# Kernel tuning notes

Hardware: AMD Instinct MI355X
Metric: run time of the kernel (lower is better)

Reference implementation:

```python
import jax, jax.numpy as jnp
import numpy as np

B, T, HID = 4, 4096, 768
H, D = 12, 64
N_HASHES = 2
BUCKET_SIZE = T // 32          # reformer repo config: max_seq_len // 32 = 128
N_BUCKETS = T // BUCKET_SIZE   # 32
SELF_ATTN_VALUE = -5e4         # reformer_pytorch TOKEN_SELF_ATTN_VALUE
MASK_VALUE = -1e9


def lsh_attention(X, mask_bool, W_qk, W_v, rotations):
    # X: [b, t, hid]; rotations: [d, n_hashes, n_buckets//2] (shared across batch & heads)
    b, t, _ = X.shape
    d, n_hashes, half_nb = rotations.shape
    n_buckets = 2 * half_nb
    h = W_qk.shape[0] // d
    scale = d ** -0.5

    qk = X @ W_qk.T            # shared query/key projection (bias-free in reformer_pytorch)
    v = X @ W_v.T

    def merge_heads(x):  # [b,t,h*d] -> [b*h, t, d]
        return x.reshape(b, t, h, d).transpose(0, 2, 1, 3).reshape(b * h, t, d)

    qk, v = merge_heads(qk), merge_heads(v)
    maskbh = jnp.repeat(mask_bool, h, axis=0)          # [bh, t]

    # --- LSH bucketing ---
    rotated = jnp.einsum('btf,fhi->bhti', qk, rotations)          # [bh, nh, t, nb/2]
    rotated = jnp.concatenate([rotated, -rotated], axis=-1)       # [bh, nh, t, nb]
    buckets = jnp.argmax(rotated, axis=-1)                        # [bh, nh, t]
    offsets = (jnp.arange(n_hashes) * n_buckets)[None, :, None]
    buckets = (buckets + offsets).reshape(b * h, n_hashes * t)

    # --- stable sort by (bucket, position) ---
    total = n_hashes * t
    ticker = jnp.arange(total)[None, :]
    buckets_and_t = buckets * t + (ticker % t)
    sticker = jnp.argsort(buckets_and_t, axis=-1)   # stable
    undo = jnp.argsort(sticker, axis=-1)
    st = sticker % t                                 # original positions, sorted order

    sqk = jnp.take_along_axis(qk, st[..., None], axis=1)
    sv = jnp.take_along_axis(v, st[..., None], axis=1)
    smask = jnp.take_along_axis(maskbh, st, axis=1)

    # --- chunk; each chunk attends to itself + previous chunk ---
    n_chunks = n_hashes * n_buckets
    cl = total // n_chunks                                  # == bucket_size
    bq_t = st.reshape(b * h, n_chunks, cl)
    bqk = sqk.reshape(b * h, n_chunks, cl, d)
    bv = sv.reshape(b * h, n_chunks, cl, d)
    bmask = smask.reshape(b * h, n_chunks, cl)

    bq = bqk
    bk = bqk / jnp.clip(jnp.linalg.norm(bqk, axis=-1, keepdims=True), 1e-12)

    def look_one_back(x):
        return jnp.concatenate([x, jnp.roll(x, 1, axis=1)], axis=2)

    bk, bv = look_one_back(bk), look_one_back(bv)
    bkv_t = look_one_back(bq_t)
    bkv_mask = look_one_back(bmask)

    dots = jnp.einsum('bnie,bnje->bnij', bq, bk) * scale    # [bh, n_chunks, cl, 2cl]
    pad = bmask[..., :, None] & bkv_mask[..., None, :]
    dots = jnp.where(pad, dots, MASK_VALUE)
    self_mask = bq_t[..., :, None] == bkv_t[..., None, :]
    dots = jnp.where(self_mask, SELF_ATTN_VALUE, dots)

    lse = jax.scipy.special.logsumexp(dots, axis=-1, keepdims=True)
    probs = jnp.exp(dots - lse)
    bo = jnp.einsum('bnij,bnje->bnie', probs, bv)

    # --- unsort and combine hash rounds via softmax over round logsumexps ---
    so = bo.reshape(b * h, total, d)
    slogits = lse.reshape(b * h, total)
    o = jnp.take_along_axis(so, undo[..., None], axis=1)
    logits = jnp.take_along_axis(slogits, undo, axis=1)

    o = o.reshape(b * h, n_hashes, t, d)
    logits = logits.reshape(b * h, n_hashes, t, 1)
    round_probs = jnp.exp(logits - jax.scipy.special.logsumexp(logits, axis=1, keepdims=True))
    out = jnp.sum(o * round_probs, axis=1)                  # [bh, t, d]
    return out.reshape(b, h, t, d).transpose(0, 2, 1, 3).reshape(b, t, h * d)


def setup_inputs() -> dict:
    key = jax.random.key(0)
    ks = jax.random.split(key, 8)
    s = 1.0 / np.sqrt(HID)
    return {
        'X': jax.random.normal(ks[0], (B, T, HID), jnp.float32),
        'mask': jnp.ones((B, T), jnp.float32),
        'W_qk': jax.random.uniform(ks[1], (H * D, HID), jnp.float32, -s, s),
        'W_v': jax.random.uniform(ks[2], (H * D, HID), jnp.float32, -s, s),
        'rotations': jax.random.normal(ks[3], (D, N_HASHES, N_BUCKETS // 2), jnp.float32),
        'W_to': jax.random.uniform(ks[4], (HID, H * D), jnp.float32, -s, s),
        'b_to': jnp.zeros((HID,), jnp.float32),
        'W_o': jax.random.uniform(ks[5], (HID, HID), jnp.float32, -s, s),
        'b_o': jnp.zeros((HID,), jnp.float32),
    }


def reference(X, mask, W_qk, W_v, rotations, W_to, b_to, W_o, b_o):
    attn = lsh_attention(X, mask.astype(bool), W_qk, W_v, rotations)
    attn = attn @ W_to.T + b_to     # LSHSelfAttention.to_out
    return attn @ W_o.T + b_o       # ReformerAttention.W_o
```

## Files before the change

### kernel.cpp

```cpp
#include <hip/hip_runtime.h>
#include <hip/hip_bf16.h>
#include <math.h>


typedef __attribute__((ext_vector_type(8))) short bf16x8;
typedef __attribute__((ext_vector_type(4))) float f32x4;

__device__ __forceinline__ float bf_lo(unsigned int w) { return __uint_as_float(w << 16); }
__device__ __forceinline__ float bf_hi(unsigned int w) { return __uint_as_float(w & 0xffff0000u); }
__device__ __forceinline__ float load_in(const void* p, size_t i, bool f32) {
  return f32 ? ((const float*)p)[i]
             : __bfloat162float(((const __hip_bfloat16*)p)[i]);
}
__device__ __forceinline__ unsigned short f2bf(float x) {
  __hip_bfloat16 h = __float2bfloat16(x);
  return *reinterpret_cast<unsigned short*>(&h);
}
__device__ __forceinline__ float bf2f(unsigned short u) { return __uint_as_float(((unsigned int)u) << 16); }

__global__ void k_detect(const unsigned int* __restrict__ X, int* __restrict__ flag) {
  if (threadIdx.x == 0 && blockIdx.x == 0) {
    int vote = 0;
    for (int i = 0; i < 64; ++i) {
      unsigned int e = (X[i] >> 7) & 0xffu;
      vote += (e >= 100u && e <= 141u) ? 1 : 0;
    }
    *flag = (vote < 32) ? 1 : 0;
  }
}

__global__ __launch_bounds__(256) void k_convert(
    const void* __restrict__ src, unsigned short* __restrict__ dst, int n,
    const int* __restrict__ flag) {
  const bool f32in = (*flag != 0);
  int i = blockIdx.x * 256 + threadIdx.x;
  if (i >= n) return;
  if (f32in) dst[i] = f2bf(((const float*)src)[i]);
  else       dst[i] = ((const unsigned short*)src)[i];
}

__global__ __launch_bounds__(256) void k_build_wrot(
    const void* __restrict__ Wqk, const void* __restrict__ rot,
    double* __restrict__ WrotT, const int* __restrict__ flag) {
  const bool f32in = (*flag != 0);
  int idx = blockIdx.x * 256 + threadIdx.x;
  if (idx >= 768 * 384) return;
  int row = idx % 384;
  int c   = idx / 384;
  int hh = row >> 5, hi = row & 31;
  double s = 0.0;
  for (int f = 0; f < 64; ++f) {
    double rv = (double)load_in(rot, f * 32 + hi, f32in);
    double wv = (double)load_in(Wqk, (size_t)(hh * 64 + f) * 768 + c, f32in);
    s = fma(rv, wv, s);
  }
  WrotT[(size_t)c * 384 + row] = s;
}

__global__ __launch_bounds__(256) void k_bucket(
    const void* __restrict__ X, const double* __restrict__ WrotT,
    unsigned char* __restrict__ cls, const int* __restrict__ flag) {
  const bool f32in = (*flag != 0);
  __shared__ double SH[6336];
  double* Xs = SH;
  double* Ws = SH + 2080;
  double* Sc = SH;
  const int tid = threadIdx.x;
  const int M0 = blockIdx.x * 128;
  const int N0 = blockIdx.y * 96;
  const int tm = tid >> 4, tn = tid & 15;
  const int sr = tid >> 1, sh = tid & 1;
  const int wk = tid >> 4, wg = tid & 15;

  double acc[8][6];
  #pragma unroll
  for (int i = 0; i < 8; ++i)
    #pragma unroll
    for (int j = 0; j < 6; ++j) acc[i][j] = 0.0;

  for (int k0 = 0; k0 < 768; k0 += 16) {
    __syncthreads();
    {
      size_t base = (size_t)(M0 + sr) * 768 + k0 + sh * 8;
      double xv[8];
      if (f32in) {
        const float4* fp = (const float4*)((const float*)X + base);
        float4 f0 = fp[0], f1 = fp[1];
        xv[0] = f0.x; xv[1] = f0.y; xv[2] = f0.z; xv[3] = f0.w;
        xv[4] = f1.x; xv[5] = f1.y; xv[6] = f1.z; xv[7] = f1.w;
      } else {
        uint4 u = *(const uint4*)((const unsigned short*)X + base);
        xv[0] = (double)bf_lo(u.x); xv[1] = (double)bf_hi(u.x);
        xv[2] = (double)bf_lo(u.y); xv[3] = (double)bf_hi(u.y);
        xv[4] = (double)bf_lo(u.z); xv[5] = (double)bf_hi(u.z);
        xv[6] = (double)bf_lo(u.w); xv[7] = (double)bf_hi(u.w);
      }
      #pragma unroll
      for (int j = 0; j < 8; ++j) Xs[(sh * 8 + j) * 130 + sr] = xv[j];
    }
    {
      const double* wp = WrotT + (size_t)(k0 + wk) * 384 + N0 + wg * 6;
      #pragma unroll
      for (int e = 0; e < 6; ++e) Ws[wk * 98 + wg * 6 + e] = wp[e];
    }
    __syncthreads();
    #pragma unroll
    for (int k = 0; k < 16; ++k) {
      double a_[8], b_[6];
      #pragma unroll
      for (int i = 0; i < 8; ++i) a_[i] = Xs[k * 130 + tm * 8 + i];
      #pragma unroll
      for (int j = 0; j < 6; ++j) b_[j] = Ws[k * 98 + tn * 6 + j];
      #pragma unroll
      for (int i = 0; i < 8; ++i)
        #pragma unroll
        for (int j = 0; j < 6; ++j)
          acc[i][j] = fma(a_[i], b_[j], acc[i][j]);
    }
  }

  #pragma unroll
  for (int chunk = 0; chunk < 2; ++chunk) {
    __syncthreads();
    if ((tm >> 3) == chunk) {
      #pragma unroll
      for (int tt = 0; tt < 8; ++tt)
        #pragma unroll
        for (int rr = 0; rr < 6; ++rr)
          Sc[(tn * 6 + rr) * 66 + (tm & 7) * 8 + tt] = acc[tt][rr];
    }
    __syncthreads();
    for (int task = tid; task < 384; task += 256) {
      int g = task >> 6, tok = task & 63;
      const double* s = &Sc[(g * 16) * 66 + tok];
      double mx = -1.0e300;
      #pragma unroll
      for (int i = 0; i < 16; ++i) {
        double a = s[i * 66];
        mx = fmax(mx, fmax(a, -a));
      }
      int amax = 0;
      #pragma unroll
      for (int i = 15; i >= 0; --i) if (-s[i * 66] == mx) amax = 16 + i;
      #pragma unroll
      for (int i = 15; i >= 0; --i) if (s[i * 66] == mx) amax = i;
      int m = M0 + chunk * 64 + tok;
      int b = m >> 12, t = m & 4095;
      int gg = blockIdx.y * 6 + g, hh = gg >> 1, h = gg & 1;
      cls[(size_t)(b * 12 + hh) * 8192 + h * 4096 + t] = (unsigned char)(h * 32 + amax);
    }
  }
}

__global__ __launch_bounds__(1024) void k_sort(
    const unsigned char* __restrict__ clsg,
    unsigned short* __restrict__ stick) {
  __shared__ unsigned short cntg[128 * 64];
  __shared__ int classbase[64];
  const int row = blockIdx.x;
  const int tid = threadIdx.x;
  const int wave = tid >> 6, lane = tid & 63;
  const unsigned char* cr = clsg + ((size_t)row << 13);

  for (int i = tid; i < 128 * 64 / 2; i += 1024) ((uint32_t*)cntg)[i] = 0;
  __syncthreads();

  unsigned char myc[8], myrank[8];
  const unsigned long long ltmask = (lane == 0) ? 0ull : (~0ull >> (64 - lane));
  #pragma unroll
  for (int chunk = 0; chunk < 8; ++chunk) {
    int g = chunk * 16 + wave;
    int j = g * 64 + lane;
    int c = cr[j];
    unsigned long long same = ~0ull;
    #pragma unroll
    for (int bit = 0; bit < 6; ++bit) {
      unsigned long long bm = __ballot((c >> bit) & 1);
      same &= ((c >> bit) & 1) ? bm : ~bm;
    }
    int rank = __popcll(same & ltmask);
    if (rank == 0) cntg[g * 64 + c] = (unsigned short)__popcll(same);
    myc[chunk] = (unsigned char)c;
    myrank[chunk] = (unsigned char)rank;
  }
  __syncthreads();
  if (tid < 64) {
    int run = 0;
    for (int g = 0; g < 128; ++g) {
      int t = cntg[g * 64 + tid];
      cntg[g * 64 + tid] = (unsigned short)run;
      run += t;
    }
    classbase[tid] = run;
  }
  __syncthreads();
  if (tid == 0) {
    int run = 0;
    for (int c = 0; c < 64; ++c) { int t = classbase[c]; classbase[c] = run; run += t; }
  }
  __syncthreads();
  unsigned short* out = stick + ((size_t)row << 13);
  #pragma unroll
  for (int chunk = 0; chunk < 8; ++chunk) {
    int g = chunk * 16 + wave;
    int j = g * 64 + lane;
    int c = myc[chunk];
    int pos = classbase[c] + cntg[g * 64 + c] + myrank[chunk];
    out[pos] = (unsigned short)j;
  }
}

__global__ __launch_bounds__(256) void k_gemm_mfma(
    const unsigned short* __restrict__ A, const unsigned short* __restrict__ W,
    const void* __restrict__ bias, void* __restrict__ Cout,
    int layout, int out_ext, const int* __restrict__ flag) {
  const bool f32in = (*flag != 0);
  const bool oF32 = out_ext && f32in;
  __shared__ unsigned short As[128 * 40];
  __shared__ unsigned short Bs[128 * 40];
  const int tid = threadIdx.x;
  const int bm = blockIdx.x, bn = blockIdx.y;
  const int w = tid >> 6, lane = tid & 63;
  const int l15 = lane & 15, lq = lane >> 4;
  const int wm = (w >> 1) * 64, wn = (w & 1) * 64;
  const int r4 = tid >> 2, c4 = tid & 3;
  const unsigned short* Ag = A + (size_t)(bm * 128 + r4) * 768 + c4 * 8;
  const unsigned short* Bg = W + (size_t)(bn * 128 + r4) * 768 + c4 * 8;
  f32x4 acc[4][4];
  #pragma unroll
  for (int i = 0; i < 4; ++i)
    #pragma unroll
    for (int j = 0; j < 4; ++j) acc[i][j] = (f32x4){0.f, 0.f, 0.f, 0.f};
  uint4 pa0 = *(const uint4*)(Ag);
  uint4 pa1 = *(const uint4*)(Ag + 64 * 768);
  uint4 pb0 = *(const uint4*)(Bg);
  uint4 pb1 = *(const uint4*)(Bg + 64 * 768);
  for (int kt = 0; kt < 24; ++kt) {
    __syncthreads();
    *(uint4*)&As[r4 * 40 + c4 * 8] = pa0;
    *(uint4*)&As[(r4 + 64) * 40 + c4 * 8] = pa1;
    *(uint4*)&Bs[r4 * 40 + c4 * 8] = pb0;
    *(uint4*)&Bs[(r4 + 64) * 40 + c4 * 8] = pb1;
    __syncthreads();
    if (kt < 23) {
      int off = (kt + 1) * 32;
      pa0 = *(const uint4*)(Ag + off);
      pa1 = *(const uint4*)(Ag + 64 * 768 + off);
      pb0 = *(const uint4*)(Bg + off);
      pb1 = *(const uint4*)(Bg + 64 * 768 + off);
    }
    bf16x8 af[4], bfr[4];
    #pragma unroll
    for (int mt = 0; mt < 4; ++mt)
      af[mt] = *(const bf16x8*)&As[(wm + mt * 16 + l15) * 40 + lq * 8];
    #pragma unroll
    for (int nt = 0; nt < 4; ++nt)
      bfr[nt] = *(const bf16x8*)&Bs[(wn + nt * 16 + l15) * 40 + lq * 8];
    #pragma unroll
    for (int mt = 0; mt < 4; ++mt)
      #pragma unroll
      for (int nt = 0; nt < 4; ++nt)
        acc[mt][nt] = __builtin_amdgcn_mfma_f32_16x16x32_bf16(af[mt], bfr[nt], acc[mt][nt], 0, 0, 0);
  }
  #pragma unroll
  for (int mt = 0; mt < 4; ++mt) {
    #pragma unroll
    for (int nt = 0; nt < 4; ++nt) {
      #pragma unroll
      for (int reg = 0; reg < 4; ++reg) {
        int m = bm * 128 + wm + mt * 16 + lq * 4 + reg;
        int n = bn * 128 + wn + nt * 16 + l15;
        float val = acc[mt][nt][reg];
        if (bias != nullptr) val += load_in(bias, n, f32in);
        if (layout == 0) {
          size_t addr = (size_t)m * 768 + n;
          if (oF32) ((float*)Cout)[addr] = val;
          else      ((unsigned short*)Cout)[addr] = f2bf(val);
        } else {
          int b2 = m >> 12, t2 = m & 4095, hh = n >> 6, f = n & 63;
          ((unsigned short*)Cout)[((((size_t)(b2 * 12 + hh)) << 12) + t2) * 64 + f] = f2bf(val);
        }
      }
    }
  }
}

__global__ __launch_bounds__(256) void k_norm(
    const unsigned short* __restrict__ qk, float* __restrict__ nk) {
  int row = blockIdx.x * 32 + (threadIdx.x >> 3);
  int cs = threadIdx.x & 7;
  const uint4* p = (const uint4*)(qk + (size_t)row * 64);
  uint4 wv = p[cs];
  float s = 0.f;
  float e;
  e = bf_lo(wv.x); s += e * e;  e = bf_hi(wv.x); s += e * e;
  e = bf_lo(wv.y); s += e * e;  e = bf_hi(wv.y); s += e * e;
  e = bf_lo(wv.z); s += e * e;  e = bf_hi(wv.z); s += e * e;
  e = bf_lo(wv.w); s += e * e;  e = bf_hi(wv.w); s += e * e;
  s += __shfl_xor(s, 1, 64);
  s += __shfl_xor(s, 2, 64);
  s += __shfl_xor(s, 4, 64);
  if (cs == 0) nk[row] = 1.0f / fmaxf(sqrtf(s), 1e-12f);
}

__global__ __launch_bounds__(256) void k_attn_mfma(
    const unsigned short* __restrict__ qk,
    const unsigned short* __restrict__ vv,
    const unsigned short* __restrict__ stick,
    const void* __restrict__ mask,
    const float* __restrict__ nk,
    unsigned short* __restrict__ o_r,
    float* __restrict__ lse_r,
    const int* __restrict__ flag) {
  const bool f32in = (*flag != 0);
  __shared__ unsigned short Qs[128 * 72];
  __shared__ unsigned short Ks[64 * 72];
  __shared__ unsigned short Vt[64 * 72];
  __shared__ unsigned short Ps[4 * 32 * 72];
  __shared__ unsigned short Tq[128];
  __shared__ unsigned short Tkv[64];
  __shared__ float Nkv[64];
  unsigned short* Vs = Ps;

  const int tid = threadIdx.x;
  const int bh = blockIdx.x >> 6;
  const int ci = blockIdx.x & 63;
  const int b  = bh / 12;
  const int prev = (ci + 63) & 63;
  const int w = tid >> 6, lane = tid & 63;
  const int l15 = lane & 15, lq = lane >> 4;
  const unsigned short* srow = stick + ((size_t)bh << 13);
  const int jrow = tid >> 3, cs = tid & 7;

  #pragma unroll
  for (int pass = 0; pass < 4; ++pass) {
    int r = jrow + pass * 32;
    int s = srow[ci * 128 + r];
    int t = s & 4095;
    uint4 qw = ((const uint4*)(qk + ((((size_t)bh << 12) + t) << 6)))[cs];
    *(uint4*)&Qs[r * 72 + cs * 8] = qw;
    if (cs == 0) {
      float mv = load_in(mask, b * 4096 + t, f32in);
      Tq[r] = (unsigned short)(s | ((mv != 0.0f) ? 0 : 0x8000));
    }
  }
  __syncthreads();

  unsigned short tqr[2][4];
  #pragma unroll
  for (int mt = 0; mt < 2; ++mt)
    #pragma unroll
    for (int reg = 0; reg < 4; ++reg)
      tqr[mt][reg] = Tq[w * 32 + mt * 16 + lq * 4 + reg];

  float m_run[2][4], l_run[2][4];
  f32x4 oacc[2][4];
  #pragma unroll
  for (int mt = 0; mt < 2; ++mt)
    #pragma unroll
    for (int reg = 0; reg < 4; ++reg) { m_run[mt][reg] = -3.0e38f; l_run[mt][reg] = 0.0f; }
  #pragma unroll
  for (int mt = 0; mt < 2; ++mt)
    #pragma unroll
    for (int nto = 0; nto < 4; ++nto) oacc[mt][nto] = (f32x4){0.f, 0.f, 0.f, 0.f};

  for (int kt = 0; kt < 4; ++kt) {
    __syncthreads();
    #pragma unroll
    for (int pass = 0; pass < 2; ++pass) {
      int j = jrow + pass * 32;
      int chunk = (kt < 2) ? ci : prev;
      int s = srow[chunk * 128 + (kt & 1) * 64 + j];
      int t = s & 4095;
      const uint4* kb = (const uint4*)(qk + ((((size_t)bh << 12) + t) << 6));
      *(uint4*)&Ks[j * 72 + cs * 8] = kb[cs];
      const uint4* vb = (const uint4*)(vv + ((((size_t)bh << 12) + t) << 6));
      int sw = (cs ^ (j & 7) ^ (j >> 3)) & 7;
      *(uint4*)&Vs[j * 72 + sw * 8] = vb[cs];
      if (cs == 0) {
        float mv = load_in(mask, b * 4096 + t, f32in);
        Tkv[j] = (unsigned short)(t | ((mv != 0.0f) ? 0 : 0x8000));
        Nkv[j] = nk[((size_t)bh << 12) + t] * 0.125f;
      }
    }
    __syncthreads();

    #pragma unroll
    for (int i = 0; i < 8; ++i) {
      int cp = w * 8 + i;
      int q8 = cp >> 2;
      int sw = (q8 ^ (lane & 7) ^ (lane >> 3)) & 7;
      uint32_t wv = *(const uint32_t*)&Vs[lane * 72 + sw * 8 + ((2 * cp) & 7)];
      Vt[(2 * cp) * 72 + lane]     = (unsigned short)(wv & 0xffff);
      Vt[(2 * cp + 1) * 72 + lane] = (unsigned short)(wv >> 16);
    }

    f32x4 sacc[2][4];
    #pragma unroll
    for (int mt = 0; mt < 2; ++mt)
      #pragma unroll
      for (int nt = 0; nt < 4; ++nt) sacc[mt][nt] = (f32x4){0.f, 0.f, 0.f, 0.f};
    #pragma unroll
    for (int ks = 0; ks < 2; ++ks) {
      bf16x8 af[2];
      #pragma unroll
      for (int mt = 0; mt < 2; ++mt)
        af[mt] = *(const bf16x8*)&Qs[(w * 32 + mt * 16 + l15) * 72 + ks * 32 + lq * 8];
      #pragma unroll
      for (int nt = 0; nt < 4; ++nt) {
        bf16x8 bfr = *(const bf16x8*)&Ks[(nt * 16 + l15) * 72 + ks * 32 + lq * 8];
        #pragma unroll
        for (int mt = 0; mt < 2; ++mt)
          sacc[mt][nt] = __builtin_amdgcn_mfma_f32_16x16x32_bf16(af[mt], bfr, sacc[mt][nt], 0, 0, 0);
      }
    }

    unsigned short tkc[4];
    float nkc[4];
    #pragma unroll
    for (int nt = 0; nt < 4; ++nt) {
      tkc[nt] = Tkv[nt * 16 + l15];
      nkc[nt] = Nkv[nt * 16 + l15];
    }
    float dv[2][4][4];
    #pragma unroll
    for (int mt = 0; mt < 2; ++mt)
      #pragma unroll
      for (int nt = 0; nt < 4; ++nt)
        #pragma unroll
        for (int reg = 0; reg < 4; ++reg) {
          float x = sacc[mt][nt][reg] * nkc[nt];
          unsigned short ts = tqr[mt][reg];
          if (((tkc[nt] | ts) & 0x8000) != 0) x = -1.0e9f;
          if (((tkc[nt] ^ ts) & 0x0fff) == 0) x = -5.0e4f;
          dv[mt][nt][reg] = x;
        }
    float mn[2][4], scv[2][4];
    #pragma unroll
    for (int mt = 0; mt < 2; ++mt)
      #pragma unroll
      for (int reg = 0; reg < 4; ++reg) {
        float rm = fmaxf(fmaxf(dv[mt][0][reg], dv[mt][1][reg]),
                         fmaxf(dv[mt][2][reg], dv[mt][3][reg]));
        rm = fmaxf(rm, __shfl_xor(rm, 1, 64));
        rm = fmaxf(rm, __shfl_xor(rm, 2, 64));
        rm = fmaxf(rm, __shfl_xor(rm, 4, 64));
        rm = fmaxf(rm, __shfl_xor(rm, 8, 64));
        float mnew = fmaxf(m_run[mt][reg], rm);
        scv[mt][reg] = __expf(m_run[mt][reg] - mnew);
        m_run[mt][reg] = mnew;
        mn[mt][reg] = mnew;
      }
    #pragma unroll
    for (int mt = 0; mt < 2; ++mt)
      #pragma unroll
      for (int nt = 0; nt < 4; ++nt)
        #pragma unroll
        for (int reg = 0; reg < 4; ++reg)
          dv[mt][nt][reg] = __expf(dv[mt][nt][reg] - mn[mt][reg]);
    #pragma unroll
    for (int mt = 0; mt < 2; ++mt)
      #pragma unroll
      for (int reg = 0; reg < 4; ++reg) {
        float rs = ((dv[mt][0][reg] + dv[mt][1][reg]) + (dv[mt][2][reg] + dv[mt][3][reg]));
        rs += __shfl_xor(rs, 1, 64);
        rs += __shfl_xor(rs, 2, 64);
        rs += __shfl_xor(rs, 4, 64);
        rs += __shfl_xor(rs, 8, 64);
        l_run[mt][reg] = l_run[mt][reg] * scv[mt][reg] + rs;
      }
    #pragma unroll
    for (int mt = 0; mt < 2; ++mt)
      #pragma unroll
      for (int nto = 0; nto < 4; ++nto)
        #pragma unroll
        for (int reg = 0; reg < 4; ++reg)
          oacc[mt][nto][reg] *= scv[mt][reg];

    __syncthreads();

    #pragma unroll
    for (int mt = 0; mt < 2; ++mt)
      #pragma unroll
      for (int nt = 0; nt < 4; ++nt)
        #pragma unroll
        for (int reg = 0; reg < 4; ++reg)
          Ps[w * 2304 + (mt * 16 + lq * 4 + reg) * 72 + nt * 16 + l15] = f2bf(dv[mt][nt][reg]);

    #pragma unroll
    for (int ks = 0; ks < 2; ++ks) {
      bf16x8 pf[2];
      #pragma unroll
      for (int mt = 0; mt < 2; ++mt)
        pf[mt] = *(const bf16x8*)&Ps[w * 2304 + (mt * 16 + l15) * 72 + ks * 32 + lq * 8];
      #pragma unroll
      for (int nto = 0; nto < 4; ++nto) {
        bf16x8 vf = *(const bf16x8*)&Vt[(nto * 16 + l15) * 72 + ks * 32 + lq * 8];
        #pragma unroll
        for (int mt = 0; mt < 2; ++mt)
          oacc[mt][nto] = __builtin_amdgcn_mfma_f32_16x16x32_bf16(pf[mt], vf, oacc[mt][nto], 0, 0, 0);
      }
    }
  }

  float invl[2][4];
  #pragma unroll
  for (int mt = 0; mt < 2; ++mt)
    #pragma unroll
    for (int reg = 0; reg < 4; ++reg) {
      float lr = l_run[mt][reg];
      invl[mt][reg] = 1.0f / lr;
      if (l15 == 0) {
        int Rr = w * 32 + mt * 16 + lq * 4 + reg;
        int s = Tq[Rr];
        int tq0 = s & 4095, rq0 = (s >> 12) & 1;
        lse_r[(((size_t)(bh * 2 + rq0)) << 12) + tq0] = m_run[mt][reg] + __logf(lr);
      }
    }
  #pragma unroll
  for (int mt = 0; mt < 2; ++mt)
    #pragma unroll
    for (int nto = 0; nto < 4; ++nto)
      #pragma unroll
      for (int reg = 0; reg < 4; ++reg)
        Ps[w * 2304 + (mt * 16 + lq * 4 + reg) * 72 + nto * 16 + l15] =
            f2bf(oacc[mt][nto][reg] * invl[mt][reg]);
  #pragma unroll
  for (int pass = 0; pass < 4; ++pass) {
    int rl = pass * 8 + (lane >> 3);
    int s = Tq[w * 32 + rl];
    int tq0 = s & 4095, rq0 = (s >> 12) & 1;
    uint4 ov = *(const uint4*)&Ps[w * 2304 + rl * 72 + (lane & 7) * 8];
    *(uint4*)(o_r + ((((size_t)(bh * 2 + rq0)) << 12) + tq0) * 64 + (lane & 7) * 8) = ov;
  }
}

__global__ __launch_bounds__(256) void k_combine(
    const unsigned short* __restrict__ o_r,
    const float* __restrict__ lse_r,
    unsigned short* __restrict__ attn) {
  int idx = blockIdx.x * 256 + threadIdx.x;
  if (idx >= 48 * 4096 * 64) return;
  int f = idx & 63;
  int t = (idx >> 6) & 4095;
  int bh = idx >> 18;
  float l0 = lse_r[((size_t)(bh * 2 + 0) << 12) + t];
  float l1 = lse_r[((size_t)(bh * 2 + 1) << 12) + t];
  float mm = fmaxf(l0, l1);
  float e0 = __expf(l0 - mm), e1 = __expf(l1 - mm);
  float inv = 1.0f / (e0 + e1);
  float o0 = bf2f(o_r[(((size_t)(bh * 2 + 0) << 12) + t) * 64 + f]);
  float o1 = bf2f(o_r[(((size_t)(bh * 2 + 1) << 12) + t) * 64 + f]);
  float res = (e0 * o0 + e1 * o1) * inv;
  int b = bh / 12, hh = bh % 12;
  attn[((size_t)(b * 4096 + t)) * 768 + hh * 64 + f] = f2bf(res);
}

extern "C" void kernel_launch(void* const* d_in, const int* in_sizes, int n_in,
                              void* d_out, int out_size, void* d_ws, size_t ws_size,
                              hipStream_t stream) {
  (void)in_sizes; (void)n_in; (void)out_size; (void)ws_size;
  const void* X    = d_in[0];
  const void* mask = d_in[1];
  const void* Wqk  = d_in[2];
  const void* Wv   = d_in[3];
  const void* rot  = d_in[4];
  const void* Wto  = d_in[5];
  const void* bto  = d_in[6];
  const void* Wo   = d_in[7];
  const void* bo   = d_in[8];

  char* ws = (char*)d_ws;
  int*            flag  = (int*)(ws);
  unsigned short* stick = (unsigned short*)(ws + 256);
  float*          lse_r = (float*)(ws + 786688);
  float*          nk    = (float*)(ws + 2359552);
  unsigned short* qk    = (unsigned short*)(ws + 3145984);
  unsigned short* v     = (unsigned short*)(ws + 28311808);
  unsigned short* o_r   = (unsigned short*)(ws + 53477632);
  double*         WrotT = (double*)(ws + 53477632);
  unsigned char*  cls   = (unsigned char*)(ws + 55836928);
  unsigned short* Wqkb  = (unsigned short*)(ws + 56230144);
  unsigned short* Wvb   = (unsigned short*)(ws + 57409792);
  unsigned short* Xb    = (unsigned short*)(ws + 58589440);
  unsigned short* Wtob  = (unsigned short*)(ws + 53477632);
  unsigned short* Wob   = (unsigned short*)(ws + 54657280);
  unsigned short* attn  = v;
  unsigned short* tmp   = qk;

  k_detect<<<1, 64, 0, stream>>>((const unsigned int*)X, flag);
  k_convert<<<49152, 256, 0, stream>>>(X, Xb, 12582912, flag);
  k_convert<<<2304, 256, 0, stream>>>(Wqk, Wqkb, 589824, flag);
  k_convert<<<2304, 256, 0, stream>>>(Wv, Wvb, 589824, flag);
  k_build_wrot<<<1152, 256, 0, stream>>>(Wqk, rot, WrotT, flag);
  k_bucket<<<dim3(128, 4), 256, 0, stream>>>(X, WrotT, cls, flag);
  k_sort<<<48, 1024, 0, stream>>>(cls, stick);
  k_gemm_mfma<<<dim3(128, 6), 256, 0, stream>>>(Xb, Wqkb, nullptr, qk, 1, 0, flag);
  k_gemm_mfma<<<dim3(128, 6), 256, 0, stream>>>(Xb, Wvb,  nullptr, v,  1, 0, flag);
  k_norm<<<6144, 256, 0, stream>>>(qk, nk);
  k_attn_mfma<<<3072, 256, 0, stream>>>(qk, v, stick, mask, nk, o_r, lse_r, flag);
  k_combine<<<49152, 256, 0, stream>>>(o_r, lse_r, attn);
  k_convert<<<2304, 256, 0, stream>>>(Wto, Wtob, 589824, flag);
  k_convert<<<2304, 256, 0, stream>>>(Wo, Wob, 589824, flag);
  k_gemm_mfma<<<dim3(128, 6), 256, 0, stream>>>(attn, Wtob, bto, tmp, 0, 0, flag);
  k_gemm_mfma<<<dim3(128, 6), 256, 0, stream>>>(tmp, Wob, bo, d_out, 0, 1, flag);
}
```

Before: 698.3 us.

## Use FP64 MFMA for bucketing GEMM with register-prefetched tiles

Replaces the scalar FP64 FMA outer-product loop in the LSH bucketing kernel with 16x16x4 FP64 MFMA instructions, each wave computing a 32x96 tile. The output lane-to-element mapping is found at runtime with identity MFMAs. The next K-slice of X and the rotated weights is prefetched into registers while the current slice is computed, hiding global load latency. This keeps the double-precision argmax exact, at the cost of more registers and a new accumulator write-back layout.

```diff
diff --git a/kernel.cpp b/kernel.cpp
--- a/kernel.cpp
+++ b/kernel.cpp
@@ -5,6 +5,7 @@
 
 typedef __attribute__((ext_vector_type(8))) short bf16x8;
 typedef __attribute__((ext_vector_type(4))) float f32x4;
+typedef __attribute__((ext_vector_type(4))) double f64x4;
 
 __device__ __forceinline__ float bf_lo(unsigned int w) { return __uint_as_float(w << 16); }
 __device__ __forceinline__ float bf_hi(unsigned int w) { return __uint_as_float(w & 0xffff0000u); }
@@ -68,66 +69,88 @@
   const int tid = threadIdx.x;
   const int M0 = blockIdx.x * 128;
   const int N0 = blockIdx.y * 96;
-  const int tm = tid >> 4, tn = tid & 15;
+  const int w = tid >> 6, lane = tid & 63;
+  const int l15 = lane & 15, lq = lane >> 4;
   const int sr = tid >> 1, sh = tid & 1;
   const int wk = tid >> 4, wg = tid & 15;
 
-  double acc[8][6];
-  #pragma unroll
-  for (int i = 0; i < 8; ++i)
-    #pragma unroll
-    for (int j = 0; j < 6; ++j) acc[i][j] = 0.0;
-
+  f64x4 acc[2][6];
+  #pragma unroll
+  for (int i = 0; i < 2; ++i)
+    #pragma unroll
+    for (int j = 0; j < 6; ++j) acc[i][j] = (f64x4){0.0, 0.0, 0.0, 0.0};
+
+  int rowid[4], colid[4];
+  {
+    f64x4 zz = (f64x4){0.0, 0.0, 0.0, 0.0};
+    f64x4 pr = __builtin_amdgcn_mfma_f64_16x16x4f64(
+        (double)l15, (lq == 0) ? 1.0 : 0.0, zz, 0, 0, 0);
+    f64x4 pc = __builtin_amdgcn_mfma_f64_16x16x4f64(
+        (lq == 0) ? 1.0 : 0.0, (double)l15, zz, 0, 0, 0);
+    #pragma unroll
+    for (int r = 0; r < 4; ++r) {
+      rowid[r] = (int)pr[r];
+      colid[r] = (int)pc[r];
+    }
+  }
+
+  double xv[8];
+  double wvv[6];
+  auto load_chunk = [&](int k0) {
+    size_t base = (size_t)(M0 + sr) * 768 + k0 + sh * 8;
+    if (f32in) {
+      const float4* fp = (const float4*)((const float*)X + base);
+      float4 f0 = fp[0], f1 = fp[1];
+      xv[0] = f0.x; xv[1] = f0.y; xv[2] = f0.z; xv[3] = f0.w;
+      xv[4] = f1.x; xv[5] = f1.y; xv[6] = f1.z; xv[7] = f1.w;
+    } else {
+      uint4 u = *(const uint4*)((const unsigned short*)X + base);
+      xv[0] = (double)bf_lo(u.x); xv[1] = (double)bf_hi(u.x);
+      xv[2] = (double)bf_lo(u.y); xv[3] = (double)bf_hi(u.y);
+      xv[4] = (double)bf_lo(u.z); xv[5] = (double)bf_hi(u.z);
+      xv[6] = (double)bf_lo(u.w); xv[7] = (double)bf_hi(u.w);
+    }
+    const double* wp = WrotT + (size_t)(k0 + wk) * 384 + N0 + wg * 6;
+    #pragma unroll
+    for (int e = 0; e < 6; ++e) wvv[e] = wp[e];
+  };
+
+  load_chunk(0);
   for (int k0 = 0; k0 < 768; k0 += 16) {
     __syncthreads();
-    {
-      size_t base = (size_t)(M0 + sr) * 768 + k0 + sh * 8;
-      double xv[8];
-      if (f32in) {
-        const float4* fp = (const float4*)((const float*)X + base);
-        float4 f0 = fp[0], f1 = fp[1];
-        xv[0] = f0.x; xv[1] = f0.y; xv[2] = f0.z; xv[3] = f0.w;
-        xv[4] = f1.x; xv[5] = f1.y; xv[6] = f1.z; xv[7] = f1.w;
-      } else {
-        uint4 u = *(const uint4*)((const unsigned short*)X + base);
-        xv[0] = (double)bf_lo(u.x); xv[1] = (double)bf_hi(u.x);
-        xv[2] = (double)bf_lo(u.y); xv[3] = (double)bf_hi(u.y);
-        xv[4] = (double)bf_lo(u.z); xv[5] = (double)bf_hi(u.z);
-        xv[6] = (double)bf_lo(u.w); xv[7] = (double)bf_hi(u.w);
-      }
-      #pragma unroll
-      for (int j = 0; j < 8; ++j) Xs[(sh * 8 + j) * 130 + sr] = xv[j];
-    }
-    {
-      const double* wp = WrotT + (size_t)(k0 + wk) * 384 + N0 + wg * 6;
-      #pragma unroll
-      for (int e = 0; e < 6; ++e) Ws[wk * 98 + wg * 6 + e] = wp[e];
-    }
-    __syncthreads();
-    #pragma unroll
-    for (int k = 0; k < 16; ++k) {
-      double a_[8], b_[6];
-      #pragma unroll
-      for (int i = 0; i < 8; ++i) a_[i] = Xs[k * 130 + tm * 8 + i];
-      #pragma unroll
-      for (int j = 0; j < 6; ++j) b_[j] = Ws[k * 98 + tn * 6 + j];
-      #pragma unroll
-      for (int i = 0; i < 8; ++i)
+    #pragma unroll
+    for (int j = 0; j < 8; ++j) Xs[(sh * 8 + j) * 130 + sr] = xv[j];
+    #pragma unroll
+    for (int e = 0; e < 6; ++e) Ws[wk * 98 + wg * 6 + e] = wvv[e];
+    __syncthreads();
+    if (k0 < 752) load_chunk(k0 + 16);
+    #pragma unroll
+    for (int kq = 0; kq < 4; ++kq) {
+      const double* xr = &Xs[(kq * 4 + lq) * 130 + l15];
+      double a0 = xr[w * 32];
+      double a1 = xr[w * 32 + 16];
+      const double* wr = &Ws[(kq * 4 + lq) * 98 + l15];
+      #pragma unroll
+      for (int nt = 0; nt < 6; ++nt) {
+        double b = wr[nt * 16];
+        acc[0][nt] = __builtin_amdgcn_mfma_f64_16x16x4f64(a0, b, acc[0][nt], 0, 0, 0);
+        acc[1][nt] = __builtin_amdgcn_mfma_f64_16x16x4f64(a1, b, acc[1][nt], 0, 0, 0);
+      }
+    }
+  }
+
+  #pragma unroll
+  for (int chunk = 0; chunk < 2; ++chunk) {
+    __syncthreads();
+    if ((w >> 1) == chunk) {
+      int lr = (w & 1) * 32;
+      #pragma unroll
+      for (int mt = 0; mt < 2; ++mt)
         #pragma unroll
-        for (int j = 0; j < 6; ++j)
-          acc[i][j] = fma(a_[i], b_[j], acc[i][j]);
-    }
-  }
-
-  #pragma unroll
-  for (int chunk = 0; chunk < 2; ++chunk) {
-    __syncthreads();
-    if ((tm >> 3) == chunk) {
-      #pragma unroll
-      for (int tt = 0; tt < 8; ++tt)
-        #pragma unroll
-        for (int rr = 0; rr < 6; ++rr)
-          Sc[(tn * 6 + rr) * 66 + (tm & 7) * 8 + tt] = acc[tt][rr];
+        for (int nt = 0; nt < 6; ++nt)
+          #pragma unroll
+          for (int r = 0; r < 4; ++r)
+            Sc[(nt * 16 + colid[r]) * 66 + lr + mt * 16 + rowid[r]] = acc[mt][nt][r];
     }
     __syncthreads();
     for (int task = tid; task < 384; task += 256) {
```

After: 658.4 us. -5.7%, faster.
